# Kernel tuning notes

Measured on AMD Instinct MI355X. Metric: run time of the kernel, lower is better.

The kernel has to match this reference:

```python
import jax, jax.numpy as jnp
import numpy as np

N_NODES = 100000


def sage_conv(x, src, dst, W_l, b_l, W_r):
    # PyG SAGEConv (aggr='mean'): out = lin_l(mean_{j->i} x_j) + lin_r(x_i)
    # lin_l has bias, lin_r does not.
    msgs = x[src]                                             # [E, d_in] irregular gather
    summed = jax.ops.segment_sum(msgs, dst, num_segments=N_NODES)
    deg = jax.ops.segment_sum(jnp.ones((src.shape[0],), x.dtype), dst,
                              num_segments=N_NODES)
    mean = summed / jnp.maximum(deg, 1.0)[:, None]            # [N, d_in]
    return mean @ W_l.T + b_l + x @ W_r.T                     # [N, d_out]


def setup_inputs() -> dict:
    key = jax.random.key(0)
    ks = jax.random.split(key, 8)
    input_dim, hidden_dim, output_dim = 64, 128, 64
    E = 1600000
    x = jax.random.normal(ks[0], (N_NODES, input_dim), dtype=jnp.float32)
    edge_index = jax.random.randint(ks[1], (2, E), 0, N_NODES, dtype=jnp.int64)

    def glorot(k, shape):
        lim = (6.0 / (shape[0] + shape[1])) ** 0.5
        return jax.random.uniform(k, shape, jnp.float32, -lim, lim)

    W1_l = glorot(ks[2], (hidden_dim, input_dim))
    b1 = jnp.zeros((hidden_dim,), jnp.float32)
    W1_r = glorot(ks[3], (hidden_dim, input_dim))
    W2_l = glorot(ks[4], (output_dim, hidden_dim))
    b2 = jnp.zeros((output_dim,), jnp.float32)
    W2_r = glorot(ks[5], (output_dim, hidden_dim))
    return {"x": x, "edge_index": edge_index,
            "W1_l": W1_l, "b1": b1, "W1_r": W1_r,
            "W2_l": W2_l, "b2": b2, "W2_r": W2_r}


def reference(x, edge_index, W1_l, b1, W1_r, W2_l, b2, W2_r):
    src, dst = edge_index[0], edge_index[1]
    h = jax.nn.relu(sage_conv(x, src, dst, W1_l, b1, W1_r))
    h = jax.nn.relu(sage_conv(h, src, dst, W2_l, b2, W2_r))
    # Original module computes norm(x) and dropout(x) but discards the results,
    # so the returned value is just the second ReLU output.
    return h
```

## Files before the change

kernel.cpp:

```cpp
#include <hip/hip_runtime.h>
#include <hip/hip_bf16.h>


#define NODE_DIM0 64
#define NPBK 512
#define MAXB 256
#define CAPB 12288
#define EPB  4096

__device__ inline unsigned short f2bf(float f) {
    unsigned u = __float_as_uint(f);
    return (unsigned short)((u + 0x7fffu + ((u >> 16) & 1u)) >> 16);
}


__global__ __launch_bounds__(256) void bucket_scatter(const int* __restrict__ src,
                                                      const int* __restrict__ dst,
                                                      int* __restrict__ gcur,
                                                      unsigned* __restrict__ pairs, int E) {
    __shared__ int hist[MAXB];
    __shared__ int incl[MAXB];
    __shared__ int exoff[MAXB];
    __shared__ int cur[MAXB];
    __shared__ int chunkBase[MAXB];
    __shared__ unsigned staged[EPB];
    __shared__ unsigned char sbkt[EPB];
    const int t = threadIdx.x;
    const int base = blockIdx.x * EPB;
    int cnt = E - base; if (cnt > EPB) cnt = EPB;

    hist[t] = 0;
    __syncthreads();

    int myS[16], myD[16];
#pragma unroll
    for (int it = 0; it < 16; ++it) {
        int e = base + it * 256 + t;
        if (e < E) {
            myS[it] = src[e];
            myD[it] = dst[e];
            atomicAdd(&hist[myD[it] >> 9], 1);
        } else {
            myD[it] = -1;
        }
    }
    __syncthreads();

    incl[t] = hist[t];
    __syncthreads();
    for (int o = 1; o < 256; o <<= 1) {
        int add = (t >= o) ? incl[t - o] : 0;
        __syncthreads();
        incl[t] += add;
        __syncthreads();
    }
    exoff[t] = incl[t] - hist[t];
    cur[t] = 0;
    chunkBase[t] = (hist[t] > 0) ? atomicAdd(&gcur[t], hist[t]) : 0;
    __syncthreads();

#pragma unroll
    for (int it = 0; it < 16; ++it) {
        if (myD[it] >= 0) {
            int b = myD[it] >> 9;
            int p = exoff[b] + atomicAdd(&cur[b], 1);
            staged[p] = ((unsigned)(myD[it] & (NPBK - 1)) << 17) | (unsigned)myS[it];
            sbkt[p] = (unsigned char)b;
        }
    }
    __syncthreads();

    for (int p = t; p < cnt; p += 256) {
        int b = sbkt[p];
        int g = chunkBase[b] + (p - exoff[b]);
        if (g < CAPB) pairs[(size_t)b * CAPB + g] = staged[p];
    }
}


__global__ __launch_bounds__(256) void bucket_csr(const unsigned* __restrict__ pairs,
                                                  const int* __restrict__ gcur,
                                                  int* __restrict__ startA,
                                                  int* __restrict__ degA,
                                                  int* __restrict__ esrc, int N) {
    __shared__ int ldeg[NPBK];
    __shared__ int scn[NPBK];
    __shared__ int lcur[NPBK];
    __shared__ int lsrc[CAPB];
    const int b = blockIdx.x;
    const int t = threadIdx.x;
    const int node0 = b * NPBK;
    int cnt = gcur[b]; if (cnt > CAPB) cnt = CAPB;

    ldeg[t] = 0; ldeg[t + 256] = 0;
    __syncthreads();

    const unsigned* reg = pairs + (size_t)b * CAPB;
    for (int i = t; i < cnt; i += 256)
        atomicAdd(&ldeg[reg[i] >> 17], 1);
    __syncthreads();

    scn[t] = ldeg[t]; scn[t + 256] = ldeg[t + 256];
    __syncthreads();
    for (int o = 1; o < NPBK; o <<= 1) {
        int a0 = (t >= o) ? scn[t - o] : 0;
        int a1 = (t + 256 >= o) ? scn[t + 256 - o] : 0;
        __syncthreads();
        scn[t] += a0; scn[t + 256] += a1;
        __syncthreads();
    }
    int e0 = scn[t] - ldeg[t];
    int e1 = scn[t + 256] - ldeg[t + 256];
    lcur[t] = e0; lcur[t + 256] = e1;
    const int gbase = b * CAPB;
    if (node0 + t < N)       { startA[node0 + t] = gbase + e0;       degA[node0 + t] = ldeg[t]; }
    if (node0 + 256 + t < N) { startA[node0 + 256 + t] = gbase + e1; degA[node0 + 256 + t] = ldeg[t + 256]; }
    __syncthreads();

    for (int i = t; i < cnt; i += 256) {
        unsigned w = reg[i];
        int pos = atomicAdd(&lcur[w >> 17], 1);
        lsrc[pos] = (int)(w & 0x1FFFFu);
    }
    __syncthreads();

    int* out = esrc + (size_t)b * CAPB;
    for (int i = t; i < cnt; i += 256) out[i] = lsrc[i];
}


__global__ void cast_bf(const float* __restrict__ in, unsigned short* __restrict__ out, int n4) {
    int i = blockIdx.x * 256 + threadIdx.x;
    if (i < n4) {
        float4 v = ((const float4*)in)[i];
        ushort4 o;
        o.x = f2bf(v.x); o.y = f2bf(v.y); o.z = f2bf(v.z); o.w = f2bf(v.w);
        ((ushort4*)out)[i] = o;
    }
}

__global__ void cast_weights(const float* __restrict__ a, const float* __restrict__ b,
                             const float* __restrict__ c, const float* __restrict__ d,
                             unsigned short* __restrict__ oa, unsigned short* __restrict__ ob,
                             unsigned short* __restrict__ oc, unsigned short* __restrict__ od) {
    int i = blockIdx.x * 256 + threadIdx.x;
    if (i < 8192) {
        oa[i] = f2bf(a[i]); ob[i] = f2bf(b[i]);
        oc[i] = f2bf(c[i]); od[i] = f2bf(d[i]);
    }
}


template <int MODE>
__global__ __launch_bounds__(256) void gather64(const unsigned short* __restrict__ feat,
                                                const int* __restrict__ startA,
                                                const int* __restrict__ degA,
                                                const int* __restrict__ esrc,
                                                const unsigned short* __restrict__ sdata,
                                                unsigned short* __restrict__ meanOut,
                                                float* __restrict__ outF, int n) {
    const int w = (blockIdx.x * 256 + threadIdx.x) >> 3;
    const int fl = threadIdx.x & 7;
    if (w >= n) return;
    const int s0 = startA[w], dg = degA[w];
    float acc[8] = {0.f, 0.f, 0.f, 0.f, 0.f, 0.f, 0.f, 0.f};
    const int* ep = esrc + s0;
    int e = 0;
    for (; e + 4 <= dg; e += 4) {
        int s_[4];
#pragma unroll
        for (int k = 0; k < 4; ++k) s_[k] = ep[e + k];
        uint4 u[4];
#pragma unroll
        for (int k = 0; k < 4; ++k)
            u[k] = *(const uint4*)(feat + (size_t)s_[k] * 64 + fl * 8);
#pragma unroll
        for (int k = 0; k < 4; ++k) {
            acc[0] += __uint_as_float(u[k].x << 16);
            acc[1] += __uint_as_float(u[k].x & 0xffff0000u);
            acc[2] += __uint_as_float(u[k].y << 16);
            acc[3] += __uint_as_float(u[k].y & 0xffff0000u);
            acc[4] += __uint_as_float(u[k].z << 16);
            acc[5] += __uint_as_float(u[k].z & 0xffff0000u);
            acc[6] += __uint_as_float(u[k].w << 16);
            acc[7] += __uint_as_float(u[k].w & 0xffff0000u);
        }
    }
    for (; e < dg; ++e) {
        uint4 u = *(const uint4*)(feat + (size_t)ep[e] * 64 + fl * 8);
        acc[0] += __uint_as_float(u.x << 16);
        acc[1] += __uint_as_float(u.x & 0xffff0000u);
        acc[2] += __uint_as_float(u.y << 16);
        acc[3] += __uint_as_float(u.y & 0xffff0000u);
        acc[4] += __uint_as_float(u.z << 16);
        acc[5] += __uint_as_float(u.z & 0xffff0000u);
        acc[6] += __uint_as_float(u.w << 16);
        acc[7] += __uint_as_float(u.w & 0xffff0000u);
    }
    const float inv = 1.0f / fmaxf((float)dg, 1.0f);
    if (MODE == 0) {
        unsigned us[8];
#pragma unroll
        for (int q = 0; q < 8; ++q) us[q] = f2bf(acc[q] * inv);
        uint4 o4;
        o4.x = us[0] | (us[1] << 16);
        o4.y = us[2] | (us[3] << 16);
        o4.z = us[4] | (us[5] << 16);
        o4.w = us[6] | (us[7] << 16);
        *(uint4*)(meanOut + (size_t)w * 64 + fl * 8) = o4;
    } else {
        uint4 us = *(const uint4*)(sdata + (size_t)w * 64 + fl * 8);
        float sv8[8];
        sv8[0] = __uint_as_float(us.x << 16);
        sv8[1] = __uint_as_float(us.x & 0xffff0000u);
        sv8[2] = __uint_as_float(us.y << 16);
        sv8[3] = __uint_as_float(us.y & 0xffff0000u);
        sv8[4] = __uint_as_float(us.z << 16);
        sv8[5] = __uint_as_float(us.z & 0xffff0000u);
        sv8[6] = __uint_as_float(us.w << 16);
        sv8[7] = __uint_as_float(us.w & 0xffff0000u);
        float4 o0, o1;
        o0.x = fmaxf(acc[0] * inv + sv8[0], 0.f);
        o0.y = fmaxf(acc[1] * inv + sv8[1], 0.f);
        o0.z = fmaxf(acc[2] * inv + sv8[2], 0.f);
        o0.w = fmaxf(acc[3] * inv + sv8[3], 0.f);
        o1.x = fmaxf(acc[4] * inv + sv8[4], 0.f);
        o1.y = fmaxf(acc[5] * inv + sv8[5], 0.f);
        o1.z = fmaxf(acc[6] * inv + sv8[6], 0.f);
        o1.w = fmaxf(acc[7] * inv + sv8[7], 0.f);
        *(float4*)(outF + (size_t)w * 64 + fl * 8)     = o0;
        *(float4*)(outF + (size_t)w * 64 + fl * 8 + 4) = o1;
    }
}


template <int IN, int OUT, int NREP>
__global__ __launch_bounds__(256) void gemm_mfma(const unsigned short* __restrict__ meanb,
                                                 const unsigned short* __restrict__ selfb,
                                                 const unsigned short* __restrict__ Wl,
                                                 const float* __restrict__ bias,
                                                 const unsigned short* __restrict__ Wr,
                                                 unsigned short* __restrict__ outp, int n) {
    using bf16x8 = __attribute__((ext_vector_type(8))) short;
    using f32x4  = __attribute__((ext_vector_type(4))) float;
    constexpr int KK = IN / 32;
    constexpr int NT = OUT / 16;
    constexpr int NG = NT / NREP;
    const int wid  = blockIdx.x * 4 + (threadIdx.x >> 6);
    const int lane = threadIdx.x & 63;
    const int row16 = lane & 15;
    const int quad  = lane >> 4;
    const int ng  = wid % NG;
    const int mt0 = wid / NG;
    const int mstride = (gridDim.x * 4) / NG;
    const int mtiles = n / 16;

    bf16x8 bl[NREP][KK], br[NREP][KK];
    float bv[NREP];
#pragma unroll
    for (int r = 0; r < NREP; ++r) {
        int ncol = (ng * NREP + r) * 16 + row16;
#pragma unroll
        for (int kk = 0; kk < KK; ++kk) {
            bl[r][kk] = *(const bf16x8*)(Wl + (size_t)ncol * IN + kk * 32 + quad * 8);
            br[r][kk] = *(const bf16x8*)(Wr + (size_t)ncol * IN + kk * 32 + quad * 8);
        }
        bv[r] = bias[ncol];
    }

    for (int mt = mt0; mt < mtiles; mt += mstride) {
        const int m = mt * 16 + row16;
        bf16x8 am[KK], as2[KK];
#pragma unroll
        for (int kk = 0; kk < KK; ++kk) {
            am[kk]  = *(const bf16x8*)(meanb + (size_t)m * IN + kk * 32 + quad * 8);
            as2[kk] = *(const bf16x8*)(selfb + (size_t)m * IN + kk * 32 + quad * 8);
        }
#pragma unroll
        for (int r = 0; r < NREP; ++r) {
            f32x4 acc = {0.f, 0.f, 0.f, 0.f};
#pragma unroll
            for (int kk = 0; kk < KK; ++kk)
                acc = __builtin_amdgcn_mfma_f32_16x16x32_bf16(am[kk], bl[r][kk], acc, 0, 0, 0);
#pragma unroll
            for (int kk = 0; kk < KK; ++kk)
                acc = __builtin_amdgcn_mfma_f32_16x16x32_bf16(as2[kk], br[r][kk], acc, 0, 0, 0);
            const int ncol = (ng * NREP + r) * 16 + row16;
            const int rowb = mt * 16 + quad * 4;
#pragma unroll
            for (int i = 0; i < 4; ++i) {
                float v = fmaxf(acc[i] + bv[r], 0.f);
                outp[(size_t)(rowb + i) * OUT + ncol] = f2bf(v);
            }
        }
    }
}


template <int IN, int OUT, int NREP>
__global__ __launch_bounds__(256) void gemm_dual2(const unsigned short* __restrict__ A,
                                                  const unsigned short* __restrict__ Wl,
                                                  const float* __restrict__ bias,
                                                  const unsigned short* __restrict__ Wr,
                                                  unsigned short* __restrict__ zout,
                                                  unsigned short* __restrict__ sout, int n) {
    using bf16x8 = __attribute__((ext_vector_type(8))) short;
    using f32x4  = __attribute__((ext_vector_type(4))) float;
    constexpr int KK = IN / 32;
    constexpr int NT = OUT / 16;
    constexpr int NG = NT / NREP;
    const int wid  = blockIdx.x * 4 + (threadIdx.x >> 6);
    const int lane = threadIdx.x & 63;
    const int row16 = lane & 15;
    const int quad  = lane >> 4;
    const int ng  = wid % NG;
    const int mt0 = wid / NG;
    const int mstride = (gridDim.x * 4) / NG;
    const int mtiles = n / 16;

    bf16x8 bl[NREP][KK], br[NREP][KK];
    float bv[NREP];
#pragma unroll
    for (int r = 0; r < NREP; ++r) {
        int ncol = (ng * NREP + r) * 16 + row16;
#pragma unroll
        for (int kk = 0; kk < KK; ++kk) {
            bl[r][kk] = *(const bf16x8*)(Wl + (size_t)ncol * IN + kk * 32 + quad * 8);
            br[r][kk] = *(const bf16x8*)(Wr + (size_t)ncol * IN + kk * 32 + quad * 8);
        }
        bv[r] = bias[ncol];
    }

    for (int mt = mt0; mt < mtiles; mt += mstride) {
        const int m = mt * 16 + row16;
        bf16x8 am[KK];
#pragma unroll
        for (int kk = 0; kk < KK; ++kk)
            am[kk] = *(const bf16x8*)(A + (size_t)m * IN + kk * 32 + quad * 8);
#pragma unroll
        for (int r = 0; r < NREP; ++r) {
            f32x4 accz = {0.f, 0.f, 0.f, 0.f};
            f32x4 accs = {0.f, 0.f, 0.f, 0.f};
#pragma unroll
            for (int kk = 0; kk < KK; ++kk) {
                accz = __builtin_amdgcn_mfma_f32_16x16x32_bf16(am[kk], bl[r][kk], accz, 0, 0, 0);
                accs = __builtin_amdgcn_mfma_f32_16x16x32_bf16(am[kk], br[r][kk], accs, 0, 0, 0);
            }
            const int ncol = (ng * NREP + r) * 16 + row16;
            const int rowb = mt * 16 + quad * 4;
#pragma unroll
            for (int i = 0; i < 4; ++i) {
                zout[(size_t)(rowb + i) * OUT + ncol] = f2bf(accz[i]);
                sout[(size_t)(rowb + i) * OUT + ncol] = f2bf(accs[i] + bv[r]);
            }
        }
    }
}


static inline char* align_up(char* p, size_t a) {
    return (char*)(((uintptr_t)p + a - 1) & ~(uintptr_t)(a - 1));
}

extern "C" void kernel_launch(void* const* d_in, const int* in_sizes, int n_in,
                              void* d_out, int out_size, void* d_ws, size_t ws_size,
                              hipStream_t stream) {
    const float* x   = (const float*)d_in[0];
    const int*   ei  = (const int*)d_in[1];
    const float* W1l = (const float*)d_in[2];
    const float* b1  = (const float*)d_in[3];
    const float* W1r = (const float*)d_in[4];
    const float* W2l = (const float*)d_in[5];
    const float* b2  = (const float*)d_in[6];
    const float* W2r = (const float*)d_in[7];
    float* out = (float*)d_out;

    const int N = in_sizes[0] / NODE_DIM0;
    const int E = in_sizes[1] / 2;
    const int* src = ei;
    const int* dst = ei + E;
    const int nbuck = (N + NPBK - 1) / NPBK;

    char* p = (char*)d_ws;
    int* gcur   = (int*)p; p += (size_t)MAXB * 4;          p = align_up(p, 16);
    int* startA = (int*)p; p += (size_t)N * 4;             p = align_up(p, 16);
    int* degA   = (int*)p; p += (size_t)N * 4;             p = align_up(p, 16);
    int* esrc   = (int*)p; p += (size_t)nbuck * CAPB * 4;  p = align_up(p, 16);
    unsigned short* xbf   = (unsigned short*)p; p += (size_t)N * 64 * 2;
    unsigned short* h1bf  = (unsigned short*)p; p += (size_t)N * 128 * 2;
    unsigned short* scr2  = (unsigned short*)p; p += (size_t)N * 128 * 2;
    unsigned short* wl1bf = (unsigned short*)p; p += (size_t)128 * 64 * 2;
    unsigned short* wr1bf = (unsigned short*)p; p += (size_t)128 * 64 * 2;
    unsigned short* wl2bf = (unsigned short*)p; p += (size_t)64 * 128 * 2;
    unsigned short* wr2bf = (unsigned short*)p; p += (size_t)64 * 128 * 2;

    unsigned* pairs = (unsigned*)scr2;
    unsigned short* meanbf = scr2;
    unsigned short* zbf = scr2;
    unsigned short* sbf = scr2 + (size_t)N * 64;

    hipMemsetAsync(gcur, 0, (size_t)MAXB * 4, stream);
    bucket_scatter<<<(E + EPB - 1) / EPB, 256, 0, stream>>>(src, dst, gcur, pairs, E);
    bucket_csr<<<nbuck, 256, 0, stream>>>(pairs, gcur, startA, degA, esrc, N);

    cast_bf<<<(N * 64 / 4 + 255) / 256, 256, 0, stream>>>(x, xbf, N * 64 / 4);
    cast_weights<<<32, 256, 0, stream>>>(W1l, W1r, W2l, W2r, wl1bf, wr1bf, wl2bf, wr2bf);

    gather64<0><<<(N * 8 + 255) / 256, 256, 0, stream>>>(xbf, startA, degA, esrc, nullptr, meanbf, nullptr, N);
    gemm_mfma<64, 128, 2><<<512, 256, 0, stream>>>(meanbf, xbf, wl1bf, b1, wr1bf, h1bf, N);

    gemm_dual2<128, 64, 2><<<512, 256, 0, stream>>>(h1bf, wl2bf, b2, wr2bf, zbf, sbf, N);
    gather64<1><<<(N * 8 + 255) / 256, 256, 0, stream>>>(zbf, startA, degA, esrc, sbf, nullptr, out, N);
}
```

Before: 228.9 us.

## Fuse layer-1 GEMM and layer-2 dual GEMM through shared-memory h1 tile

Merges the layer-1 SAGE linear (mean and self projections with ReLU) and the layer-2 dual projection into one kernel. The 16-row h1 tile is staged in LDS instead of being written to and re-read from global memory, which removes a kernel launch and a round trip of N×128 bf16 through HBM. The gather loop is also unrolled from 4 to 8 edges to keep more loads in flight. In exchange each tile iteration now needs two block barriers, and the mean buffer gets its own workspace allocation.

```diff
diff --git a/kernel.cpp b/kernel.cpp
--- a/kernel.cpp
+++ b/kernel.cpp
@@ -166,16 +166,16 @@
     float acc[8] = {0.f, 0.f, 0.f, 0.f, 0.f, 0.f, 0.f, 0.f};
     const int* ep = esrc + s0;
     int e = 0;
-    for (; e + 4 <= dg; e += 4) {
-        int s_[4];
-#pragma unroll
-        for (int k = 0; k < 4; ++k) s_[k] = ep[e + k];
-        uint4 u[4];
-#pragma unroll
-        for (int k = 0; k < 4; ++k)
+    for (; e + 8 <= dg; e += 8) {
+        int s_[8];
+#pragma unroll
+        for (int k = 0; k < 8; ++k) s_[k] = ep[e + k];
+        uint4 u[8];
+#pragma unroll
+        for (int k = 0; k < 8; ++k)
             u[k] = *(const uint4*)(feat + (size_t)s_[k] * 64 + fl * 8);
 #pragma unroll
-        for (int k = 0; k < 4; ++k) {
+        for (int k = 0; k < 8; ++k) {
             acc[0] += __uint_as_float(u[k].x << 16);
             acc[1] += __uint_as_float(u[k].x & 0xffff0000u);
             acc[2] += __uint_as_float(u[k].y << 16);
@@ -234,126 +234,88 @@
 }
 
 
-template <int IN, int OUT, int NREP>
-__global__ __launch_bounds__(256) void gemm_mfma(const unsigned short* __restrict__ meanb,
+__global__ __launch_bounds__(256) void fused_l12(const unsigned short* __restrict__ meanb,
                                                  const unsigned short* __restrict__ selfb,
-                                                 const unsigned short* __restrict__ Wl,
-                                                 const float* __restrict__ bias,
-                                                 const unsigned short* __restrict__ Wr,
-                                                 unsigned short* __restrict__ outp, int n) {
+                                                 const unsigned short* __restrict__ W1l,
+                                                 const float* __restrict__ b1,
+                                                 const unsigned short* __restrict__ W1r,
+                                                 const unsigned short* __restrict__ W2l,
+                                                 const float* __restrict__ b2,
+                                                 const unsigned short* __restrict__ W2r,
+                                                 unsigned short* __restrict__ zout,
+                                                 unsigned short* __restrict__ sout, int n) {
     using bf16x8 = __attribute__((ext_vector_type(8))) short;
     using f32x4  = __attribute__((ext_vector_type(4))) float;
-    constexpr int KK = IN / 32;
-    constexpr int NT = OUT / 16;
-    constexpr int NG = NT / NREP;
-    const int wid  = blockIdx.x * 4 + (threadIdx.x >> 6);
+    constexpr int LDW = 136;
+    __shared__ unsigned short h1t[16 * LDW];
+    const int wv   = threadIdx.x >> 6;
     const int lane = threadIdx.x & 63;
     const int row16 = lane & 15;
     const int quad  = lane >> 4;
-    const int ng  = wid % NG;
-    const int mt0 = wid / NG;
-    const int mstride = (gridDim.x * 4) / NG;
+
+    bf16x8 bl1[2][2], br1[2][2];
+    float bv1[2];
+#pragma unroll
+    for (int r = 0; r < 2; ++r) {
+        int nc = (wv * 2 + r) * 16 + row16;
+#pragma unroll
+        for (int kk = 0; kk < 2; ++kk) {
+            bl1[r][kk] = *(const bf16x8*)(W1l + (size_t)nc * 64 + kk * 32 + quad * 8);
+            br1[r][kk] = *(const bf16x8*)(W1r + (size_t)nc * 64 + kk * 32 + quad * 8);
+        }
+        bv1[r] = b1[nc];
+    }
+    const int nc2 = wv * 16 + row16;
+    bf16x8 bl2[4], br2[4];
+#pragma unroll
+    for (int kk = 0; kk < 4; ++kk) {
+        bl2[kk] = *(const bf16x8*)(W2l + (size_t)nc2 * 128 + kk * 32 + quad * 8);
+        br2[kk] = *(const bf16x8*)(W2r + (size_t)nc2 * 128 + kk * 32 + quad * 8);
+    }
+    const float bv2 = b2[nc2];
+
     const int mtiles = n / 16;
-
-    bf16x8 bl[NREP][KK], br[NREP][KK];
-    float bv[NREP];
-#pragma unroll
-    for (int r = 0; r < NREP; ++r) {
-        int ncol = (ng * NREP + r) * 16 + row16;
-#pragma unroll
-        for (int kk = 0; kk < KK; ++kk) {
-            bl[r][kk] = *(const bf16x8*)(Wl + (size_t)ncol * IN + kk * 32 + quad * 8);
-            br[r][kk] = *(const bf16x8*)(Wr + (size_t)ncol * IN + kk * 32 + quad * 8);
-        }
-        bv[r] = bias[ncol];
-    }
-
-    for (int mt = mt0; mt < mtiles; mt += mstride) {
+    for (int mt = blockIdx.x; mt < mtiles; mt += gridDim.x) {
         const int m = mt * 16 + row16;
-        bf16x8 am[KK], as2[KK];
-#pragma unroll
-        for (int kk = 0; kk < KK; ++kk) {
-            am[kk]  = *(const bf16x8*)(meanb + (size_t)m * IN + kk * 32 + quad * 8);
-            as2[kk] = *(const bf16x8*)(selfb + (size_t)m * IN + kk * 32 + quad * 8);
-        }
-#pragma unroll
-        for (int r = 0; r < NREP; ++r) {
+        bf16x8 am[2], as2[2];
+#pragma unroll
+        for (int kk = 0; kk < 2; ++kk) {
+            am[kk]  = *(const bf16x8*)(meanb + (size_t)m * 64 + kk * 32 + quad * 8);
+            as2[kk] = *(const bf16x8*)(selfb + (size_t)m * 64 + kk * 32 + quad * 8);
+        }
+#pragma unroll
+        for (int r = 0; r < 2; ++r) {
             f32x4 acc = {0.f, 0.f, 0.f, 0.f};
 #pragma unroll
-            for (int kk = 0; kk < KK; ++kk)
-                acc = __builtin_amdgcn_mfma_f32_16x16x32_bf16(am[kk], bl[r][kk], acc, 0, 0, 0);
-#pragma unroll
-            for (int kk = 0; kk < KK; ++kk)
-                acc = __builtin_amdgcn_mfma_f32_16x16x32_bf16(as2[kk], br[r][kk], acc, 0, 0, 0);
-            const int ncol = (ng * NREP + r) * 16 + row16;
-            const int rowb = mt * 16 + quad * 4;
-#pragma unroll
-            for (int i = 0; i < 4; ++i) {
-                float v = fmaxf(acc[i] + bv[r], 0.f);
-                outp[(size_t)(rowb + i) * OUT + ncol] = f2bf(v);
-            }
-        }
-    }
-}
-
-
-template <int IN, int OUT, int NREP>
-__global__ __launch_bounds__(256) void gemm_dual2(const unsigned short* __restrict__ A,
-                                                  const unsigned short* __restrict__ Wl,
-                                                  const float* __restrict__ bias,
-                                                  const unsigned short* __restrict__ Wr,
-                                                  unsigned short* __restrict__ zout,
-                                                  unsigned short* __restrict__ sout, int n) {
-    using bf16x8 = __attribute__((ext_vector_type(8))) short;
-    using f32x4  = __attribute__((ext_vector_type(4))) float;
-    constexpr int KK = IN / 32;
-    constexpr int NT = OUT / 16;
-    constexpr int NG = NT / NREP;
-    const int wid  = blockIdx.x * 4 + (threadIdx.x >> 6);
-    const int lane = threadIdx.x & 63;
-    const int row16 = lane & 15;
-    const int quad  = lane >> 4;
-    const int ng  = wid % NG;
-    const int mt0 = wid / NG;
-    const int mstride = (gridDim.x * 4) / NG;
-    const int mtiles = n / 16;
-
-    bf16x8 bl[NREP][KK], br[NREP][KK];
-    float bv[NREP];
-#pragma unroll
-    for (int r = 0; r < NREP; ++r) {
-        int ncol = (ng * NREP + r) * 16 + row16;
-#pragma unroll
-        for (int kk = 0; kk < KK; ++kk) {
-            bl[r][kk] = *(const bf16x8*)(Wl + (size_t)ncol * IN + kk * 32 + quad * 8);
-            br[r][kk] = *(const bf16x8*)(Wr + (size_t)ncol * IN + kk * 32 + quad * 8);
-        }
-        bv[r] = bias[ncol];
-    }
-
-    for (int mt = mt0; mt < mtiles; mt += mstride) {
-        const int m = mt * 16 + row16;
-        bf16x8 am[KK];
-#pragma unroll
-        for (int kk = 0; kk < KK; ++kk)
-            am[kk] = *(const bf16x8*)(A + (size_t)m * IN + kk * 32 + quad * 8);
-#pragma unroll
-        for (int r = 0; r < NREP; ++r) {
-            f32x4 accz = {0.f, 0.f, 0.f, 0.f};
-            f32x4 accs = {0.f, 0.f, 0.f, 0.f};
-#pragma unroll
-            for (int kk = 0; kk < KK; ++kk) {
-                accz = __builtin_amdgcn_mfma_f32_16x16x32_bf16(am[kk], bl[r][kk], accz, 0, 0, 0);
-                accs = __builtin_amdgcn_mfma_f32_16x16x32_bf16(am[kk], br[r][kk], accs, 0, 0, 0);
-            }
-            const int ncol = (ng * NREP + r) * 16 + row16;
-            const int rowb = mt * 16 + quad * 4;
-#pragma unroll
-            for (int i = 0; i < 4; ++i) {
-                zout[(size_t)(rowb + i) * OUT + ncol] = f2bf(accz[i]);
-                sout[(size_t)(rowb + i) * OUT + ncol] = f2bf(accs[i] + bv[r]);
-            }
-        }
+            for (int kk = 0; kk < 2; ++kk)
+                acc = __builtin_amdgcn_mfma_f32_16x16x32_bf16(am[kk], bl1[r][kk], acc, 0, 0, 0);
+#pragma unroll
+            for (int kk = 0; kk < 2; ++kk)
+                acc = __builtin_amdgcn_mfma_f32_16x16x32_bf16(as2[kk], br1[r][kk], acc, 0, 0, 0);
+            const int nc = (wv * 2 + r) * 16 + row16;
+#pragma unroll
+            for (int i = 0; i < 4; ++i)
+                h1t[(quad * 4 + i) * LDW + nc] = f2bf(fmaxf(acc[i] + bv1[r], 0.f));
+        }
+        __syncthreads();
+        bf16x8 a2[4];
+#pragma unroll
+        for (int kk = 0; kk < 4; ++kk)
+            a2[kk] = *(const bf16x8*)(h1t + row16 * LDW + kk * 32 + quad * 8);
+        f32x4 accz = {0.f, 0.f, 0.f, 0.f};
+        f32x4 accs = {0.f, 0.f, 0.f, 0.f};
+#pragma unroll
+        for (int kk = 0; kk < 4; ++kk) {
+            accz = __builtin_amdgcn_mfma_f32_16x16x32_bf16(a2[kk], bl2[kk], accz, 0, 0, 0);
+            accs = __builtin_amdgcn_mfma_f32_16x16x32_bf16(a2[kk], br2[kk], accs, 0, 0, 0);
+        }
+        const int rowb = mt * 16 + quad * 4;
+#pragma unroll
+        for (int i = 0; i < 4; ++i) {
+            zout[(size_t)(rowb + i) * 64 + nc2] = f2bf(accz[i]);
+            sout[(size_t)(rowb + i) * 64 + nc2] = f2bf(accs[i] + bv2);
+        }
+        __syncthreads();
     }
 }
 
@@ -387,15 +349,14 @@
     int* degA   = (int*)p; p += (size_t)N * 4;             p = align_up(p, 16);
     int* esrc   = (int*)p; p += (size_t)nbuck * CAPB * 4;  p = align_up(p, 16);
     unsigned short* xbf   = (unsigned short*)p; p += (size_t)N * 64 * 2;
-    unsigned short* h1bf  = (unsigned short*)p; p += (size_t)N * 128 * 2;
     unsigned short* scr2  = (unsigned short*)p; p += (size_t)N * 128 * 2;
     unsigned short* wl1bf = (unsigned short*)p; p += (size_t)128 * 64 * 2;
     unsigned short* wr1bf = (unsigned short*)p; p += (size_t)128 * 64 * 2;
     unsigned short* wl2bf = (unsigned short*)p; p += (size_t)64 * 128 * 2;
     unsigned short* wr2bf = (unsigned short*)p; p += (size_t)64 * 128 * 2;
+    unsigned short* meanbf = (unsigned short*)p; p += (size_t)N * 64 * 2;
 
     unsigned* pairs = (unsigned*)scr2;
-    unsigned short* meanbf = scr2;
     unsigned short* zbf = scr2;
     unsigned short* sbf = scr2 + (size_t)N * 64;
 
@@ -407,8 +368,9 @@
     cast_weights<<<32, 256, 0, stream>>>(W1l, W1r, W2l, W2r, wl1bf, wr1bf, wl2bf, wr2bf);
 
     gather64<0><<<(N * 8 + 255) / 256, 256, 0, stream>>>(xbf, startA, degA, esrc, nullptr, meanbf, nullptr, N);
-    gemm_mfma<64, 128, 2><<<512, 256, 0, stream>>>(meanbf, xbf, wl1bf, b1, wr1bf, h1bf, N);
-
-    gemm_dual2<128, 64, 2><<<512, 256, 0, stream>>>(h1bf, wl2bf, b2, wr2bf, zbf, sbf, N);
+
+    fused_l12<<<1024, 256, 0, stream>>>(meanbf, xbf, wl1bf, b1, wr1bf,
+                                        wl2bf, b2, wr2bf, zbf, sbf, N);
+
     gather64<1><<<(N * 8 + 255) / 256, 256, 0, stream>>>(zbf, startA, degA, esrc, sbf, nullptr, out, N);
 }
```

After: 228.1 us. About the same (-0.3%).
